# Kernel optimization log

Hardware: AMD Instinct MI355X
Metric: run time of the kernel (lower is better)

Reference implementation:

```python
import jax, jax.numpy as jnp
import numpy as np


def setup_inputs() -> dict:
    key = jax.random.key(0)
    k1, _ = jax.random.split(key)
    N, H, CH, T = 4, 8, 64, 2048
    qkv = jax.random.normal(k1, (N, H * 3 * CH, T), dtype=jnp.float32)
    rescale = jnp.ones((1,), dtype=jnp.float32)
    return {"qkv": qkv, "rescale": rescale, "n_heads": H}


def reference(qkv, rescale, n_heads):
    bs, width, length = qkv.shape
    ch = width // (3 * n_heads)
    # [N, H*3*C, T] -> [N*H, 3*C, T] -> three [N*H, C, T]
    qkv_h = qkv.reshape(bs * n_heads, 3 * ch, length)
    q, k, v = qkv_h[:, :ch], qkv_h[:, ch:2 * ch], qkv_h[:, 2 * ch:]
    scale = 1.0 / jnp.sqrt(jnp.sqrt(jnp.float32(ch)))
    # scores: [B*H, T, S]
    weight = jnp.einsum('bct,bcs->bts', q * scale, k * scale)
    weight = jax.nn.softmax(weight.astype(jnp.float32) * rescale[0], axis=-1).astype(qkv.dtype)
    a = jnp.einsum('bts,bcs->bct', weight, v)  # [B*H, C, T]
    return a.reshape(bs, n_heads * ch, length)
```

## Files before the change

### kernel.cpp

```cpp
#include <hip/hip_runtime.h>

typedef _Float16 half8 __attribute__((ext_vector_type(8)));
typedef _Float16 half4 __attribute__((ext_vector_type(4)));
typedef float    floatx4 __attribute__((ext_vector_type(4)));

#define T_LEN 2048
#define CH 64
#define BH 32
#define QTILE 128
#define STILE 64
#define LDP 72

__global__ __launch_bounds__(256, 2)
void attn_kernel(const float* __restrict__ qkv, const float* __restrict__ rescale,
                 float* __restrict__ out)
{
    __shared__ _Float16 Qs[QTILE][LDP];
    __shared__ _Float16 Ks[STILE][LDP];
    __shared__ _Float16 Vs[CH][LDP];
    __shared__ _Float16 Pt[4][32][LDP];

    const int tid  = threadIdx.x;
    const int wave = tid >> 6;
    const int lane = tid & 63;
    const int l15  = lane & 15;
    const int quad = lane >> 4;

    const int bh = blockIdx.y;
    const int t0 = blockIdx.x * QTILE;

    const float* qp = qkv + (size_t)(bh >> 3) * (1536 * T_LEN)
                          + (size_t)(bh & 7) * (192 * T_LEN);
    const float* kp = qp + 64 * T_LEN;
    const float* vp = qp + 128 * T_LEN;
    float* op = out + (size_t)bh * (CH * T_LEN);

    const float fscale = 0.125f * rescale[0];

    {
        const int t4 = (tid & 31) * 4;
        const int c0 = (tid >> 5) * 4;
#pragma unroll
        for (int pass = 0; pass < 2; ++pass) {
            const int c4 = c0 + pass * 32;
            float4 rr[4];
#pragma unroll
            for (int i = 0; i < 4; ++i)
                rr[i] = *(const float4*)(qp + (size_t)(c4 + i) * T_LEN + t0 + t4);
#pragma unroll
            for (int j = 0; j < 4; ++j) {
                half4 h;
                h[0] = (_Float16)((&rr[0].x)[j]);
                h[1] = (_Float16)((&rr[1].x)[j]);
                h[2] = (_Float16)((&rr[2].x)[j]);
                h[3] = (_Float16)((&rr[3].x)[j]);
                *(half4*)&Qs[t4 + j][c4] = h;
            }
        }
    }
    __syncthreads();

    half8 bq[2][2];
#pragma unroll
    for (int tb = 0; tb < 2; ++tb)
#pragma unroll
        for (int ks = 0; ks < 2; ++ks)
            bq[tb][ks] = *(const half8*)&Qs[wave * 32 + tb * 16 + l15][ks * 32 + quad * 8];

    const floatx4 fzero = {0.f, 0.f, 0.f, 0.f};
    floatx4 oacc[4][2];
#pragma unroll
    for (int mt = 0; mt < 4; ++mt)
#pragma unroll
        for (int tb = 0; tb < 2; ++tb) oacc[mt][tb] = fzero;
    float lsum[2] = {0.f, 0.f};

    for (int s0 = 0; s0 < T_LEN; s0 += STILE) {
        __syncthreads();

        {
            const int s4 = (tid & 15) * 4;
            const int c4 = (tid >> 4) * 4;
            float4 rr[4];
#pragma unroll
            for (int i = 0; i < 4; ++i)
                rr[i] = *(const float4*)(kp + (size_t)(c4 + i) * T_LEN + s0 + s4);
#pragma unroll
            for (int j = 0; j < 4; ++j) {
                half4 h;
                h[0] = (_Float16)((&rr[0].x)[j]);
                h[1] = (_Float16)((&rr[1].x)[j]);
                h[2] = (_Float16)((&rr[2].x)[j]);
                h[3] = (_Float16)((&rr[3].x)[j]);
                *(half4*)&Ks[s4 + j][c4] = h;
            }
        }
        {
            const int s4 = (tid & 15) * 4;
            const int cv = tid >> 4;
#pragma unroll
            for (int i = 0; i < 4; ++i) {
                const int c = cv + 16 * i;
                float4 r = *(const float4*)(vp + (size_t)c * T_LEN + s0 + s4);
                half4 h;
                h[0] = (_Float16)r.x; h[1] = (_Float16)r.y;
                h[2] = (_Float16)r.z; h[3] = (_Float16)r.w;
                *(half4*)&Vs[c][s4] = h;
            }
        }
        __syncthreads();

        half8 ak[4][2];
#pragma unroll
        for (int mt = 0; mt < 4; ++mt)
#pragma unroll
            for (int ks = 0; ks < 2; ++ks)
                ak[mt][ks] = *(const half8*)&Ks[mt * 16 + l15][ks * 32 + quad * 8];

        floatx4 sacc[4][2];
#pragma unroll
        for (int mt = 0; mt < 4; ++mt)
#pragma unroll
            for (int tb = 0; tb < 2; ++tb) sacc[mt][tb] = fzero;

#pragma unroll
        for (int mt = 0; mt < 4; ++mt)
#pragma unroll
            for (int tb = 0; tb < 2; ++tb)
#pragma unroll
                for (int ks = 0; ks < 2; ++ks)
                    sacc[mt][tb] = __builtin_amdgcn_mfma_f32_16x16x32_f16(
                        ak[mt][ks], bq[tb][ks], sacc[mt][tb], 0, 0, 0);

#pragma unroll
        for (int mt = 0; mt < 4; ++mt)
#pragma unroll
            for (int tb = 0; tb < 2; ++tb) {
                half4 ph;
#pragma unroll
                for (int r = 0; r < 4; ++r) {
                    float p = __expf(sacc[mt][tb][r] * fscale);
                    lsum[tb] += p;
                    ph[r] = (_Float16)p;
                }
                *(half4*)&Pt[wave][tb * 16 + l15][mt * 16 + quad * 4] = ph;
            }
        asm volatile("s_waitcnt lgkmcnt(0)" ::: "memory");

        half8 av[4][2], bp[2][2];
#pragma unroll
        for (int mt = 0; mt < 4; ++mt)
#pragma unroll
            for (int ks = 0; ks < 2; ++ks)
                av[mt][ks] = *(const half8*)&Vs[mt * 16 + l15][ks * 32 + quad * 8];
#pragma unroll
        for (int tb = 0; tb < 2; ++tb)
#pragma unroll
            for (int ks = 0; ks < 2; ++ks)
                bp[tb][ks] = *(const half8*)&Pt[wave][tb * 16 + l15][ks * 32 + quad * 8];

#pragma unroll
        for (int mt = 0; mt < 4; ++mt)
#pragma unroll
            for (int tb = 0; tb < 2; ++tb)
#pragma unroll
                for (int ks = 0; ks < 2; ++ks)
                    oacc[mt][tb] = __builtin_amdgcn_mfma_f32_16x16x32_f16(
                        av[mt][ks], bp[tb][ks], oacc[mt][tb], 0, 0, 0);
    }

#pragma unroll
    for (int tb = 0; tb < 2; ++tb) {
        lsum[tb] += __shfl_xor(lsum[tb], 16);
        lsum[tb] += __shfl_xor(lsum[tb], 32);
    }
    const float linv[2] = {1.0f / lsum[0], 1.0f / lsum[1]};

#pragma unroll
    for (int mt = 0; mt < 4; ++mt)
#pragma unroll
        for (int tb = 0; tb < 2; ++tb) {
            const int t = t0 + wave * 32 + tb * 16 + l15;
#pragma unroll
            for (int r = 0; r < 4; ++r) {
                const int c = mt * 16 + quad * 4 + r;
                op[(size_t)c * T_LEN + t] = oacc[mt][tb][r] * linv[tb];
            }
        }
}

extern "C" void kernel_launch(void* const* d_in, const int* in_sizes, int n_in,
                              void* d_out, int out_size, void* d_ws, size_t ws_size,
                              hipStream_t stream) {
    const float* qkv     = (const float*)d_in[0];
    const float* rescale = (const float*)d_in[1];
    float* out = (float*)d_out;
    dim3 grid(T_LEN / QTILE, BH);
    attn_kernel<<<grid, dim3(256), 0, stream>>>(qkv, rescale, out);
}
```

Before: 154.9 us.

## Pre-pack Q/K/V into fp16 MFMA fragment layout in a separate prep kernel

Adds a prep kernel that converts Q, K and V once to fp16 and stores them in the workspace in the exact per-lane MFMA fragment order. The attention kernel then loads K and V fragments straight from global memory (L2-resident) instead of repeating the fp32 loads, conversion, LDS staging and two block barriers on every S tile. The PV product is transposed so each lane owns contiguous t values, which allows float4 output stores. The cost is an extra launch and workspace traffic, and the attention loop gets no software prefetch to hide global latency.

After: 152.1 us. No clear change (-1.8%).

```diff
diff --git a/kernel.cpp b/kernel.cpp
--- a/kernel.cpp
+++ b/kernel.cpp
@@ -8,16 +8,80 @@
 #define CH 64
 #define BH 32
 #define QTILE 128
-#define STILE 64
 #define LDP 72
+#define FRAG_BH 131072
 
 __global__ __launch_bounds__(256, 2)
-void attn_kernel(const float* __restrict__ qkv, const float* __restrict__ rescale,
+void prep_kernel(const float* __restrict__ qkv, _Float16* __restrict__ ws)
+{
+    __shared__ _Float16 Qs[64][LDP];
+    __shared__ _Float16 Ks[64][LDP];
+    __shared__ _Float16 Vs[64][LDP];
+
+    const int tid  = threadIdx.x;
+    const int bh   = blockIdx.y;
+    const int tile = blockIdx.x;
+    const int x0   = tile * 64;
+
+    const float* qp = qkv + (size_t)(bh >> 3) * (1536 * T_LEN)
+                          + (size_t)(bh & 7) * (192 * T_LEN);
+    const float* kp = qp + 64 * T_LEN;
+    const float* vp = qp + 128 * T_LEN;
+
+    {
+        const int a4 = (tid & 15) * 4;
+        const int c4 = (tid >> 4) * 4;
+        float4 rq[4], rk[4];
+#pragma unroll
+        for (int i = 0; i < 4; ++i) {
+            rq[i] = *(const float4*)(qp + (size_t)(c4 + i) * T_LEN + x0 + a4);
+            rk[i] = *(const float4*)(kp + (size_t)(c4 + i) * T_LEN + x0 + a4);
+        }
+#pragma unroll
+        for (int j = 0; j < 4; ++j) {
+            half4 hq, hk;
+#pragma unroll
+            for (int i = 0; i < 4; ++i) {
+                hq[i] = (_Float16)((&rq[i].x)[j]);
+                hk[i] = (_Float16)((&rk[i].x)[j]);
+            }
+            *(half4*)&Qs[a4 + j][c4] = hq;
+            *(half4*)&Ks[a4 + j][c4] = hk;
+        }
+        const int s4 = (tid & 15) * 4;
+        const int cv = tid >> 4;
+#pragma unroll
+        for (int i = 0; i < 4; ++i) {
+            const int c = cv + 16 * i;
+            float4 r = *(const float4*)(vp + (size_t)c * T_LEN + x0 + s4);
+            half4 h; h[0]=(_Float16)r.x; h[1]=(_Float16)r.y; h[2]=(_Float16)r.z; h[3]=(_Float16)r.w;
+            *(half4*)&Vs[c][s4] = h;
+        }
+    }
+    __syncthreads();
+
+    const int lane = tid & 63, wave = tid >> 6;
+    const int l15 = lane & 15, quad = lane >> 4;
+    _Float16* qf = ws;
+    _Float16* kf = ws + (size_t)BH * FRAG_BH;
+    _Float16* vf = ws + (size_t)2 * BH * FRAG_BH;
+
+#pragma unroll
+    for (int ks = 0; ks < 2; ++ks) {
+        half8 hq = *(const half8*)&Qs[wave * 16 + l15][ks * 32 + quad * 8];
+        half8 hk = *(const half8*)&Ks[wave * 16 + l15][ks * 32 + quad * 8];
+        half8 hv = *(const half8*)&Vs[wave * 16 + l15][ks * 32 + quad * 8];
+        const size_t gqk = (((size_t)bh * 128 + tile * 4 + wave) * 2 + ks) * 512 + lane * 8;
+        *(half8*)(qf + gqk) = hq;
+        *(half8*)(kf + gqk) = hk;
+        *(half8*)(vf + (((size_t)bh * 32 + tile) * 8 + wave * 2 + ks) * 512 + lane * 8) = hv;
+    }
+}
+
+__global__ __launch_bounds__(256, 2)
+void attn_kernel(const _Float16* __restrict__ ws, const float* __restrict__ rescale,
                  float* __restrict__ out)
 {
-    __shared__ _Float16 Qs[QTILE][LDP];
-    __shared__ _Float16 Ks[STILE][LDP];
-    __shared__ _Float16 Vs[CH][LDP];
     __shared__ _Float16 Pt[4][32][LDP];
 
     const int tid  = threadIdx.x;
@@ -29,100 +93,53 @@
     const int bh = blockIdx.y;
     const int t0 = blockIdx.x * QTILE;
 
-    const float* qp = qkv + (size_t)(bh >> 3) * (1536 * T_LEN)
-                          + (size_t)(bh & 7) * (192 * T_LEN);
-    const float* kp = qp + 64 * T_LEN;
-    const float* vp = qp + 128 * T_LEN;
+    const _Float16* qf = ws;
+    const _Float16* kf = ws + (size_t)BH * FRAG_BH;
+    const _Float16* vf = ws + (size_t)2 * BH * FRAG_BH;
     float* op = out + (size_t)bh * (CH * T_LEN);
 
     const float fscale = 0.125f * rescale[0];
 
-    {
-        const int t4 = (tid & 31) * 4;
-        const int c0 = (tid >> 5) * 4;
-#pragma unroll
-        for (int pass = 0; pass < 2; ++pass) {
-            const int c4 = c0 + pass * 32;
-            float4 rr[4];
-#pragma unroll
-            for (int i = 0; i < 4; ++i)
-                rr[i] = *(const float4*)(qp + (size_t)(c4 + i) * T_LEN + t0 + t4);
-#pragma unroll
-            for (int j = 0; j < 4; ++j) {
-                half4 h;
-                h[0] = (_Float16)((&rr[0].x)[j]);
-                h[1] = (_Float16)((&rr[1].x)[j]);
-                h[2] = (_Float16)((&rr[2].x)[j]);
-                h[3] = (_Float16)((&rr[3].x)[j]);
-                *(half4*)&Qs[t4 + j][c4] = h;
-            }
-        }
-    }
-    __syncthreads();
-
     half8 bq[2][2];
 #pragma unroll
     for (int tb = 0; tb < 2; ++tb)
 #pragma unroll
         for (int ks = 0; ks < 2; ++ks)
-            bq[tb][ks] = *(const half8*)&Qs[wave * 32 + tb * 16 + l15][ks * 32 + quad * 8];
+            bq[tb][ks] = *(const half8*)(qf +
+                (((size_t)bh * 128 + (t0 >> 4) + wave * 2 + tb) * 2 + ks) * 512 + lane * 8);
 
     const floatx4 fzero = {0.f, 0.f, 0.f, 0.f};
-    floatx4 oacc[4][2];
-#pragma unroll
-    for (int mt = 0; mt < 4; ++mt)
-#pragma unroll
-        for (int tb = 0; tb < 2; ++tb) oacc[mt][tb] = fzero;
+    floatx4 oacc[2][4];
+#pragma unroll
+    for (int tb = 0; tb < 2; ++tb)
+#pragma unroll
+        for (int ct = 0; ct < 4; ++ct) oacc[tb][ct] = fzero;
     float lsum[2] = {0.f, 0.f};
 
-    for (int s0 = 0; s0 < T_LEN; s0 += STILE) {
-        __syncthreads();
-
-        {
-            const int s4 = (tid & 15) * 4;
-            const int c4 = (tid >> 4) * 4;
-            float4 rr[4];
-#pragma unroll
-            for (int i = 0; i < 4; ++i)
-                rr[i] = *(const float4*)(kp + (size_t)(c4 + i) * T_LEN + s0 + s4);
-#pragma unroll
-            for (int j = 0; j < 4; ++j) {
-                half4 h;
-                h[0] = (_Float16)((&rr[0].x)[j]);
-                h[1] = (_Float16)((&rr[1].x)[j]);
-                h[2] = (_Float16)((&rr[2].x)[j]);
-                h[3] = (_Float16)((&rr[3].x)[j]);
-                *(half4*)&Ks[s4 + j][c4] = h;
-            }
-        }
-        {
-            const int s4 = (tid & 15) * 4;
-            const int cv = tid >> 4;
-#pragma unroll
-            for (int i = 0; i < 4; ++i) {
-                const int c = cv + 16 * i;
-                float4 r = *(const float4*)(vp + (size_t)c * T_LEN + s0 + s4);
-                half4 h;
-                h[0] = (_Float16)r.x; h[1] = (_Float16)r.y;
-                h[2] = (_Float16)r.z; h[3] = (_Float16)r.w;
-                *(half4*)&Vs[c][s4] = h;
-            }
-        }
-        __syncthreads();
-
+    const _Float16* kfp = kf + (size_t)bh * FRAG_BH + lane * 8;
+    const _Float16* vfp = vf + (size_t)bh * FRAG_BH + lane * 8;
+
+    for (int st = 0; st < 32; ++st) {
         half8 ak[4][2];
 #pragma unroll
         for (int mt = 0; mt < 4; ++mt)
 #pragma unroll
             for (int ks = 0; ks < 2; ++ks)
-                ak[mt][ks] = *(const half8*)&Ks[mt * 16 + l15][ks * 32 + quad * 8];
+                ak[mt][ks] = *(const half8*)(kfp + (size_t)(mt * 2 + ks) * 512);
+        half8 bv[4][2];
+#pragma unroll
+        for (int ct = 0; ct < 4; ++ct)
+#pragma unroll
+            for (int ks = 0; ks < 2; ++ks)
+                bv[ct][ks] = *(const half8*)(vfp + (size_t)(ct * 2 + ks) * 512);
+        kfp += 4096;
+        vfp += 4096;
 
         floatx4 sacc[4][2];
 #pragma unroll
         for (int mt = 0; mt < 4; ++mt)
 #pragma unroll
             for (int tb = 0; tb < 2; ++tb) sacc[mt][tb] = fzero;
-
 #pragma unroll
         for (int mt = 0; mt < 4; ++mt)
 #pragma unroll
@@ -147,45 +164,47 @@
             }
         asm volatile("s_waitcnt lgkmcnt(0)" ::: "memory");
 
-        half8 av[4][2], bp[2][2];
-#pragma unroll
-        for (int mt = 0; mt < 4; ++mt)
+        half8 ap[2][2];
+#pragma unroll
+        for (int tb = 0; tb < 2; ++tb)
 #pragma unroll
             for (int ks = 0; ks < 2; ++ks)
-                av[mt][ks] = *(const half8*)&Vs[mt * 16 + l15][ks * 32 + quad * 8];
+                ap[tb][ks] = *(const half8*)&Pt[wave][tb * 16 + l15][ks * 32 + quad * 8];
+
 #pragma unroll
         for (int tb = 0; tb < 2; ++tb)
 #pragma unroll
-            for (int ks = 0; ks < 2; ++ks)
-                bp[tb][ks] = *(const half8*)&Pt[wave][tb * 16 + l15][ks * 32 + quad * 8];
-
-#pragma unroll
-        for (int mt = 0; mt < 4; ++mt)
-#pragma unroll
-            for (int tb = 0; tb < 2; ++tb)
+            for (int ct = 0; ct < 4; ++ct)
 #pragma unroll
                 for (int ks = 0; ks < 2; ++ks)
-                    oacc[mt][tb] = __builtin_amdgcn_mfma_f32_16x16x32_f16(
-                        av[mt][ks], bp[tb][ks], oacc[mt][tb], 0, 0, 0);
+                    oacc[tb][ct] = __builtin_amdgcn_mfma_f32_16x16x32_f16(
+                        ap[tb][ks], bv[ct][ks], oacc[tb][ct], 0, 0, 0);
     }
 
 #pragma unroll
     for (int tb = 0; tb < 2; ++tb) {
         lsum[tb] += __shfl_xor(lsum[tb], 16);
         lsum[tb] += __shfl_xor(lsum[tb], 32);
-    }
-    const float linv[2] = {1.0f / lsum[0], 1.0f / lsum[1]};
-
-#pragma unroll
-    for (int mt = 0; mt < 4; ++mt)
-#pragma unroll
-        for (int tb = 0; tb < 2; ++tb) {
-            const int t = t0 + wave * 32 + tb * 16 + l15;
-#pragma unroll
-            for (int r = 0; r < 4; ++r) {
-                const int c = mt * 16 + quad * 4 + r;
-                op[(size_t)c * T_LEN + t] = oacc[mt][tb][r] * linv[tb];
-            }
+        lsum[tb] = 1.0f / lsum[tb];
+    }
+    float linv[2][4];
+#pragma unroll
+    for (int tb = 0; tb < 2; ++tb)
+#pragma unroll
+        for (int r = 0; r < 4; ++r)
+            linv[tb][r] = __shfl(lsum[tb], quad * 4 + r);
+
+#pragma unroll
+    for (int tb = 0; tb < 2; ++tb)
+#pragma unroll
+        for (int ct = 0; ct < 4; ++ct) {
+            const int c = ct * 16 + l15;
+            const int t = t0 + wave * 32 + tb * 16 + quad * 4;
+            float4 o;
+#pragma unroll
+            for (int r = 0; r < 4; ++r)
+                (&o.x)[r] = oacc[tb][ct][r] * linv[tb][r];
+            *(float4*)(op + (size_t)c * T_LEN + t) = o;
         }
 }
 
@@ -195,6 +214,8 @@
     const float* qkv     = (const float*)d_in[0];
     const float* rescale = (const float*)d_in[1];
     float* out = (float*)d_out;
-    dim3 grid(T_LEN / QTILE, BH);
-    attn_kernel<<<grid, dim3(256), 0, stream>>>(qkv, rescale, out);
+    _Float16* ws = (_Float16*)d_ws;
+
+    prep_kernel<<<dim3(32, BH), dim3(256), 0, stream>>>(qkv, ws);
+    attn_kernel<<<dim3(T_LEN / QTILE, BH), dim3(256), 0, stream>>>(ws, rescale, out);
 }
```
